# Kernel optimization log

Hardware: AMD Instinct MI355X
Metric: run time of the kernel (lower is better)

## Reference

```python
import jax, jax.numpy as jnp
import numpy as np

N, L, N_KNOTS = 512, 64, 9
N_BINS = N_KNOTS - 1
TWO_PI = 2.0 * np.pi


def _circular_conv(x, w, b):
    # x: (N,C,H,W), w: (O,C,3,3); circular (periodic) padding as used for gauge lattices
    xp = jnp.pad(x, ((0, 0), (0, 0), (1, 1), (1, 1)), mode='wrap')
    y = jax.lax.conv_general_dilated(xp, w, (1, 1), 'VALID',
                                     dimension_numbers=('NCHW', 'OIHW', 'NCHW'))
    return y + b[None, :, None, None]


def setup_inputs() -> dict:
    key = jax.random.key(0)
    k1, k2, k3 = jax.random.split(key, 3)
    x = jax.random.normal(k1, (N, L, L), dtype=jnp.float32)
    # partition the lattice into active/passive/frozen masks
    pat = (np.add.outer(np.arange(L), 2 * np.arange(L)) % 3)
    mask_active = jnp.asarray((pat == 0).astype(np.float32))
    mask_passive = jnp.asarray((pat == 1).astype(np.float32))
    mask_frozen = jnp.asarray((pat == 2).astype(np.float32))
    conv1_w = 0.1 * jax.random.normal(k2, (32, 2, 3, 3), dtype=jnp.float32)
    conv1_b = jnp.zeros((32,), jnp.float32)
    conv2_w = 0.1 * jax.random.normal(k3, (3 * N_BINS + 1, 32, 3, 3), dtype=jnp.float32)
    conv2_b = jnp.zeros((3 * N_BINS + 1,), jnp.float32)
    return {"x": x, "mask_active": mask_active, "mask_passive": mask_passive,
            "mask_frozen": mask_frozen, "conv1_w": conv1_w, "conv1_b": conv1_b,
            "conv2_w": conv2_w, "conv2_b": conv2_b}


def reference(x, mask_active, mask_passive, mask_frozen, conv1_w, conv1_b, conv2_w, conv2_b):
    nb = N_BINS
    # prepare_u1_input: frozen-masked (cos, sin) channels
    net_in = mask_frozen[None, None] * jnp.stack([jnp.cos(x), jnp.sin(x)], axis=1)  # (N,2,L,L)
    h1 = jax.nn.gelu(_circular_conv(net_in, conv1_w, conv1_b))
    net_out = _circular_conv(h1, conv2_w, conv2_b)              # (N,3nb+1,L,L)
    net_out = jnp.transpose(net_out, (0, 2, 3, 1))              # (N,L,L,3nb+1)
    w = jax.nn.softmax(net_out[..., :nb], axis=-1)
    h = jax.nn.softmax(net_out[..., nb:2 * nb], axis=-1)
    d = jax.nn.softplus(net_out[..., 2 * nb:3 * nb])
    t = net_out[..., -1]
    # circular knots on [0, 2pi]; periodic derivative: s[-1] = s[0]
    zeros = jnp.zeros(w.shape[:-1] + (1,), w.dtype)
    kx = jnp.concatenate([zeros, TWO_PI * jnp.cumsum(w, -1)], -1)   # (N,L,L,n_knots)
    ky = jnp.concatenate([zeros, TWO_PI * jnp.cumsum(h, -1)], -1)
    s = jnp.concatenate([d, d[..., :1]], -1)
    # dir = 0 (forward): x1 = active * mod(x)
    x1 = mask_active[None] * jnp.remainder(x, TWO_PI)
    # bin search over interior knots -> k in [0, nb-1]
    k = jnp.sum((x1[..., None] >= kx[..., 1:-1]).astype(jnp.int32), axis=-1)
    g = lambda a, i: jnp.take_along_axis(a, i[..., None], axis=-1)[..., 0]
    kxk, kxk1 = g(kx, k), g(kx, k + 1)
    kyk, kyk1 = g(ky, k), g(ky, k + 1)
    sk, sk1 = g(s, k), g(s, k + 1)
    wk = kxk1 - kxk
    hk = kyk1 - kyk
    slope = hk / wk
    xi = jnp.clip((x1 - kxk) / wk, 0.0, 1.0)
    om = 1.0 - xi
    # rational-quadratic spline (Durkan et al. 2019)
    den = slope + (sk1 + sk - 2.0 * slope) * xi * om
    y = kyk + hk * (slope * xi * xi + sk * xi * om) / den
    local_logJ = jnp.log(slope * slope * (sk1 * xi * xi + 2.0 * slope * xi * om + sk * om * om)) \
                 - 2.0 * jnp.log(den)
    fx1 = mask_active[None] * (y + t)              # (1-dir)*t with dir=0
    local_logJ = mask_active[None] * local_logJ
    logJ = jnp.sum(local_logJ, axis=(1, 2))
    fx = mask_active[None] * jnp.remainder(fx1, TWO_PI) + mask_passive[None] * x + mask_frozen[None] * x
    return fx, logJ
```

## Files before the change

kernel.cpp:

```cpp
#include <hip/hip_runtime.h>
#include <math.h>

#define Nn 512
#define Ld 64
#define NB 8
#define C1 32
#define C2 25

__device__ __forceinline__ float gelu_fast(float a) {
    float a3 = a * a * a;
    float u2 = 1.5957691216057308f * (a + 0.044715f * a3);
    return a / (1.0f + __expf(-u2));
}

__device__ __forceinline__ float softplus_f(float v) {
    return (v > 0.0f) ? v + log1pf(expf(-v)) : log1pf(expf(v));
}

__device__ __forceinline__ float pos_mod_2pi(float v) {
    const float T = 6.2831853071795864769f;
    float r = fmodf(v, T);
    if (r < 0.0f) r += T;
    return r;
}

#define FCH 8
#define ISTR 67
#define IROWS 16
#define HPLANE 896

#define H1SLOT(S, B, V)                                                   \
    if (V) {                                                              \
        float vv[18];                                                     \
        _Pragma("unroll")                                                 \
        for (int di = 0; di < 3; ++di)                                    \
            _Pragma("unroll")                                             \
            for (int dj = 0; dj < 3; ++dj) {                              \
                int a = (B) + di * ISTR + dj;                             \
                vv[di * 3 + dj]     = s_cos[a];                           \
                vv[9 + di * 3 + dj] = s_sin[a];                           \
            }                                                             \
        _Pragma("unroll")                                                 \
        for (int c = 0; c < FCH; ++c) {                                   \
            const float* w = c1w + (c0 + c) * 18;     \
            float a1 = c1b[c0 + c];                                       \
            _Pragma("unroll")                                             \
            for (int t = 0; t < 9; ++t) {        \
                a1 = fmaf(vv[t],     w[t],     a1);                       \
                a1 = fmaf(vv[9 + t], w[9 + t], a1);                       \
            }                                                             \
            s_h1[c * HPLANE + (S)] = gelu_fast(a1);                       \
        }                                                                 \
    }

#define CONV2(CBASE)                                                      \
    {                                                                     \
        _Pragma("unroll 1")                                               \
        for (int c = 0; c < FCH; ++c) {                                   \
            const int eb = c * HPLANE;                                    \
            float v0 = s_h1[eb + ex0];                                    \
            float v1 = s_h1[eb + ex1];                                    \
            float v2 = s_h1[eb + ex2];                                    \
            float v3 = s_h1[eb + ex0 + 64];                               \
            float v4 = s_h1[eb + ex1 + 64];                               \
            float v5 = s_h1[eb + ex2 + 64];                               \
            float v6 = s_h1[eb + ex0 + 128];                              \
            float v7 = s_h1[eb + ex1 + 128];                              \
            float v8 = s_h1[eb + ex2 + 128];                              \
            const float* wpc = c2w + ((CBASE) + c) * 9;                   \
            _Pragma("unroll")                                             \
            for (int co = 0; co < C2; ++co) {                             \
                const float* w = wpc + co * (C1 * 9);        \
                float a2 = acc[co];                                       \
                a2 = fmaf(v0, w[0], a2);                                  \
                a2 = fmaf(v1, w[1], a2);                                  \
                a2 = fmaf(v2, w[2], a2);                                  \
                a2 = fmaf(v3, w[3], a2);                                  \
                a2 = fmaf(v4, w[4], a2);                                  \
                a2 = fmaf(v5, w[5], a2);                                  \
                a2 = fmaf(v6, w[6], a2);                                  \
                a2 = fmaf(v7, w[7], a2);                                  \
                a2 = fmaf(v8, w[8], a2);                                  \
                acc[co] = a2;                                             \
            }                                                             \
        }                                                                 \
    }

__global__ __launch_bounds__(256, 4) void csplaq_fused_kernel(
    const float* __restrict__ x,
    const float* __restrict__ c1w, const float* __restrict__ c1b,
    const float* __restrict__ c2w, const float* __restrict__ c2b,
    float* __restrict__ out_fx, float* __restrict__ out_logJ)
{
    __shared__ float s_cos[IROWS * ISTR];
    __shared__ float s_sin[IROWS * ISTR];
    __shared__ float s_h1[FCH * HPLANE];
    __shared__ float s_red[4];

    const float TWO_PI_F = 6.2831853071795864769f;

    const int tid  = threadIdx.x;
    const int band = blockIdx.x;
    const int n    = blockIdx.y;
    const int r0   = band * 12;
    const int R    = (band == 5) ? 4 : 12;
    const int rows_in = R + 4;
    const int rows_l  = R + 2;
    const int nsh     = rows_l * 64;
    const int n_active = (R == 12) ? 256 : 86;
    const float* xn = x + n * 4096;

    for (int idx = tid; idx < rows_in * 66; idx += 256) {
        int li = idx / 66, u = idx - li * 66;
        int gi = (r0 - 2 + li) & 63;
        int gj = (u - 1) & 63;
        float xv = xn[gi * 64 + gj];
        int pat = (gi + 2 * gj) % 3;
        float sv, cv;
        sincosf(xv, &sv, &cv);
        float fz = (pat == 2) ? 1.0f : 0.0f;
        s_cos[li * ISTR + u] = fz * cv;
        s_sin[li * ISTR + u] = fz * sv;
    }

    int g3 = tid >> 6, u = tid & 63;
    int rsel  = (u >= 22) + (u >= 43);
    int ubase = (rsel == 2) ? 43 : ((rsel == 1) ? 22 : 0);
    int rr = 3 * g3 + rsel;
    int cc = 3 * (u - ubase) + rsel;
    bool is_act = (tid < n_active);
    int jm = (cc + 63) & 63, jp = (cc + 1) & 63;

    const int ex0 = rr * 64 + jm, ex1 = rr * 64 + cc, ex2 = rr * 64 + jp;

    const int sA = tid, sB = tid + 256, sC = tid + 512, sD = tid + 768;
    const int bA = (sA >> 6) * ISTR + (sA & 63);
    const int bB = (sB >> 6) * ISTR + (sB & 63);
    const int bC = (sC >> 6) * ISTR + (sC & 63);
    const int bD = (sD >> 6) * ISTR + (sD & 63);
    const bool vA = (sA < nsh), vB = (sB < nsh), vC = (sC < nsh), vD = (sD < nsh);

    float acc[C2];
    #pragma unroll
    for (int co = 0; co < C2; ++co) acc[co] = c2b[co];

    #pragma unroll 1
    for (int c0 = 0; c0 < C1; c0 += FCH) {
        __syncthreads();
        H1SLOT(sA, bA, vA)
        H1SLOT(sB, bB, vB)
        H1SLOT(sC, bC, vC)
        H1SLOT(sD, bD, vD)
        __syncthreads();
        if (is_act) CONV2(c0)
    }

    float* outn = out_fx + n * 4096;
    for (int idx = tid; idx < R * 64; idx += 256) {
        int lr = idx >> 6, c = idx & 63;
        int gi = r0 + lr;
        int pat = (gi + 2 * c) % 3;
        float xv = xn[gi * 64 + c];
        if (pat != 0) outn[gi * 64 + c] = xv;
    }

    float lj_val = 0.0f;
    if (is_act) {
        int gi = r0 + rr;
        float xv = xn[gi * 64 + cc];

        float kx[NB + 1], ky[NB + 1], sar[NB + 1];
        {
            float m = acc[0];
            #pragma unroll
            for (int qi = 1; qi < NB; ++qi) m = fmaxf(m, acc[qi]);
            float e[NB], ssum = 0.0f;
            #pragma unroll
            for (int qi = 0; qi < NB; ++qi) { e[qi] = expf(acc[qi] - m); ssum += e[qi]; }
            float inv = TWO_PI_F / ssum;
            float run = 0.0f;
            kx[0] = 0.0f;
            #pragma unroll
            for (int qi = 0; qi < NB; ++qi) { run += e[qi]; kx[qi + 1] = run * inv; }
        }
        {
            float m = acc[NB];
            #pragma unroll
            for (int qi = 1; qi < NB; ++qi) m = fmaxf(m, acc[NB + qi]);
            float e[NB], ssum = 0.0f;
            #pragma unroll
            for (int qi = 0; qi < NB; ++qi) { e[qi] = expf(acc[NB + qi] - m); ssum += e[qi]; }
            float inv = TWO_PI_F / ssum;
            float run = 0.0f;
            ky[0] = 0.0f;
            #pragma unroll
            for (int qi = 0; qi < NB; ++qi) { run += e[qi]; ky[qi + 1] = run * inv; }
        }
        #pragma unroll
        for (int qi = 0; qi < NB; ++qi) sar[qi] = softplus_f(acc[2 * NB + qi]);
        sar[NB] = sar[0];
        float t_out = acc[3 * NB];

        float x1 = pos_mod_2pi(xv);
        int k = 0;
        #pragma unroll
        for (int qi = 1; qi <= NB - 1; ++qi) k += (x1 >= kx[qi]) ? 1 : 0;

        float kxk = 0.f, kxk1 = 0.f, kyk = 0.f, kyk1 = 0.f, sk = 0.f, sk1 = 0.f;
        #pragma unroll
        for (int qi = 0; qi <= NB; ++qi) {
            if (qi == k)     { kxk = kx[qi];  kyk = ky[qi];  sk  = sar[qi]; }
            if (qi == k + 1) { kxk1 = kx[qi]; kyk1 = ky[qi]; sk1 = sar[qi]; }
        }

        float wk = kxk1 - kxk;
        float hk = kyk1 - kyk;
        float slope = hk / wk;
        float xi = (x1 - kxk) / wk;
        xi = fminf(fmaxf(xi, 0.0f), 1.0f);
        float om = 1.0f - xi;
        float den = slope + (sk1 + sk - 2.0f * slope) * xi * om;
        float y = kyk + hk * (slope * xi * xi + sk * xi * om) / den;
        float num = slope * slope * (sk1 * xi * xi + 2.0f * slope * xi * om + sk * om * om);
        lj_val = logf(num) - 2.0f * logf(den);

        outn[gi * 64 + cc] = pos_mod_2pi(y + t_out);
    }

    float r = lj_val;
    #pragma unroll
    for (int off = 32; off > 0; off >>= 1) r += __shfl_down(r, off, 64);
    int lane = tid & 63, wv = tid >> 6;
    if (lane == 0) s_red[wv] = r;
    __syncthreads();
    if (tid == 0)
        atomicAdd(&out_logJ[n], s_red[0] + s_red[1] + s_red[2] + s_red[3]);
}

extern "C" void kernel_launch(void* const* d_in, const int* in_sizes, int n_in,
                              void* d_out, int out_size, void* d_ws, size_t ws_size,
                              hipStream_t stream) {
    const float* x   = (const float*)d_in[0];
    const float* c1w = (const float*)d_in[4];
    const float* c1b = (const float*)d_in[5];
    const float* c2w = (const float*)d_in[6];
    const float* c2b = (const float*)d_in[7];

    float* out_fx   = (float*)d_out;
    float* out_logJ = out_fx + (size_t)Nn * Ld * Ld;

    hipMemsetAsync(out_logJ, 0, Nn * sizeof(float), stream);

    dim3 grid(6, Nn);
    csplaq_fused_kernel<<<grid, 256, 0, stream>>>(x, c1w, c1b, c2w, c2b,
                                                  out_fx, out_logJ);
}
```

Before: 387.6 us.

## Retile into 16-row bands with 384-thread blocks and handle active-site phase

Each block now covers 16 output rows instead of 12, and the grid drops from 6 to 4 bands per sample. This removes the uneven 4-row tail band and lowers the halo recompute of conv1 relative to useful rows. Blocks grow to 384 threads and the conv1 channel chunk shrinks from 8 to 4 to fit shared memory, so there are more barrier rounds per block. Because band starts are no longer multiples of 3, the mapping of threads to active sites now accounts for the row phase, and one wave is left only partly used.

```diff
diff --git a/kernel.cpp b/kernel.cpp
--- a/kernel.cpp
+++ b/kernel.cpp
@@ -24,13 +24,16 @@
     return r;
 }
 
-#define FCH 8
+#define BTH 384
+#define RB 16
+#define FCH 4
 #define ISTR 67
-#define IROWS 16
-#define HPLANE 896
-
-#define H1SLOT(S, B, V)                                                   \
-    if (V) {                                                              \
+#define IROWS 20
+#define HROWS 18
+#define HPLANE (HROWS * 64)
+
+#define H1SLOT(S, B)                                                      \
+    {                                                                     \
         float vv[18];                                                     \
         _Pragma("unroll")                                                 \
         for (int di = 0; di < 3; ++di)                                    \
@@ -86,7 +89,7 @@
         }                                                                 \
     }
 
-__global__ __launch_bounds__(256, 4) void csplaq_fused_kernel(
+__global__ __launch_bounds__(BTH, 7) void csplaq_fused_kernel(
     const float* __restrict__ x,
     const float* __restrict__ c1w, const float* __restrict__ c1b,
     const float* __restrict__ c2w, const float* __restrict__ c2b,
@@ -95,22 +98,17 @@
     __shared__ float s_cos[IROWS * ISTR];
     __shared__ float s_sin[IROWS * ISTR];
     __shared__ float s_h1[FCH * HPLANE];
-    __shared__ float s_red[4];
+    __shared__ float s_red[6];
 
     const float TWO_PI_F = 6.2831853071795864769f;
 
     const int tid  = threadIdx.x;
     const int band = blockIdx.x;
     const int n    = blockIdx.y;
-    const int r0   = band * 12;
-    const int R    = (band == 5) ? 4 : 12;
-    const int rows_in = R + 4;
-    const int rows_l  = R + 2;
-    const int nsh     = rows_l * 64;
-    const int n_active = (R == 12) ? 256 : 86;
+    const int r0   = band * RB;
     const float* xn = x + n * 4096;
 
-    for (int idx = tid; idx < rows_in * 66; idx += 256) {
+    for (int idx = tid; idx < IROWS * 66; idx += BTH) {
         int li = idx / 66, u = idx - li * 66;
         int gi = (r0 - 2 + li) & 63;
         int gj = (u - 1) & 63;
@@ -123,22 +121,35 @@
         s_sin[li * ISTR + u] = fz * sv;
     }
 
-    int g3 = tid >> 6, u = tid & 63;
-    int rsel  = (u >= 22) + (u >= 43);
-    int ubase = (rsel == 2) ? 43 : ((rsel == 1) ? 22 : 0);
-    int rr = 3 * g3 + rsel;
-    int cc = 3 * (u - ubase) + rsel;
-    bool is_act = (tid < n_active);
-    int jm = (cc + 63) & 63, jp = (cc + 1) & 63;
+    const int g3 = tid >> 6, u = tid & 63;
+    const int rho = r0 % 3;
+    const int k22 = (3 - rho) % 3;
+    const int n0 = (k22 == 0) ? 22 : 21;
+    const int n1 = (k22 == 1) ? 22 : 21;
+    const int b1 = n0, b2 = n0 + n1;
+    int rr, cc;
+    bool is_act;
+    if (g3 < 5) {
+        int rsel  = (u >= b1) + (u >= b2);
+        int ubase = (rsel == 2) ? b2 : ((rsel == 1) ? b1 : 0);
+        rr = 3 * g3 + rsel;
+        int cres = rho + rsel; if (cres > 2) cres -= 3;
+        cc = 3 * (u - ubase) + cres;
+        is_act = true;
+    } else {
+        int m = tid - 320;
+        rr = 15;
+        cc = 3 * m + rho;
+        is_act = (m < ((rho == 0) ? 22 : 21));
+    }
+    const int jm = (cc + 63) & 63, jp = (cc + 1) & 63;
 
     const int ex0 = rr * 64 + jm, ex1 = rr * 64 + cc, ex2 = rr * 64 + jp;
 
-    const int sA = tid, sB = tid + 256, sC = tid + 512, sD = tid + 768;
+    const int sA = tid, sB = tid + BTH, sC = tid + 2 * BTH;
     const int bA = (sA >> 6) * ISTR + (sA & 63);
     const int bB = (sB >> 6) * ISTR + (sB & 63);
     const int bC = (sC >> 6) * ISTR + (sC & 63);
-    const int bD = (sD >> 6) * ISTR + (sD & 63);
-    const bool vA = (sA < nsh), vB = (sB < nsh), vC = (sC < nsh), vD = (sD < nsh);
 
     float acc[C2];
     #pragma unroll
@@ -147,16 +158,15 @@
     #pragma unroll 1
     for (int c0 = 0; c0 < C1; c0 += FCH) {
         __syncthreads();
-        H1SLOT(sA, bA, vA)
-        H1SLOT(sB, bB, vB)
-        H1SLOT(sC, bC, vC)
-        H1SLOT(sD, bD, vD)
+        H1SLOT(sA, bA)
+        H1SLOT(sB, bB)
+        H1SLOT(sC, bC)
         __syncthreads();
         if (is_act) CONV2(c0)
     }
 
     float* outn = out_fx + n * 4096;
-    for (int idx = tid; idx < R * 64; idx += 256) {
+    for (int idx = tid; idx < RB * 64; idx += BTH) {
         int lr = idx >> 6, c = idx & 63;
         int gi = r0 + lr;
         int pat = (gi + 2 * c) % 3;
@@ -234,7 +244,8 @@
     if (lane == 0) s_red[wv] = r;
     __syncthreads();
     if (tid == 0)
-        atomicAdd(&out_logJ[n], s_red[0] + s_red[1] + s_red[2] + s_red[3]);
+        atomicAdd(&out_logJ[n], s_red[0] + s_red[1] + s_red[2] +
+                                s_red[3] + s_red[4] + s_red[5]);
 }
 
 extern "C" void kernel_launch(void* const* d_in, const int* in_sizes, int n_in,
@@ -251,7 +262,7 @@
 
     hipMemsetAsync(out_logJ, 0, Nn * sizeof(float), stream);
 
-    dim3 grid(6, Nn);
-    csplaq_fused_kernel<<<grid, 256, 0, stream>>>(x, c1w, c1b, c2w, c2b,
+    dim3 grid(4, Nn);
+    csplaq_fused_kernel<<<grid, BTH, 0, stream>>>(x, c1w, c1b, c2w, c2b,
                                                   out_fx, out_logJ);
 }
```

Result: slower. 477.4 us (+23.2%).
